# Kernel optimization log

Hardware: AMD Instinct MI355X
Metric: run time of the kernel (lower is better)

Reference implementation:

```python
import jax, jax.numpy as jnp
import numpy as np

N_IN = 1024
N_OUT = 1024
L, B = 2048, 16


def setup_inputs() -> dict:
    key = jax.random.key(0)
    k1, k2 = jax.random.split(key, 2)
    val = (3.0 / N_IN) ** 0.5  # matches init_weight uniform range
    return {
        "x": jax.random.normal(k1, (L, B, N_IN), dtype=jnp.float32),
        "c0": jnp.zeros((B, N_OUT), dtype=jnp.float32),
        "weight": jax.random.uniform(k2, (N_IN, 3 * N_OUT), dtype=jnp.float32, minval=-val, maxval=val),
        "bias": jnp.zeros((2 * N_OUT,), dtype=jnp.float32),
    }


def reference(x, c0, weight, bias):
    # x: (L, B, n_in); weight: (n_in, 3*n_out); bias: (2*n_out,)
    Lx, Bx, _ = x.shape
    # u_ = x @ W, viewed as (L, B, n_out, k=3); bidir=1 dropped
    u = (x.reshape(Lx * Bx, N_IN) @ weight).reshape(Lx, Bx, N_OUT, 3)
    x_tilde = u[..., 0]                                  # (L, B, d)
    forget = jax.nn.sigmoid(u[..., 1] + bias[:N_OUT])    # (L, B, d)
    # sequential SRU recurrence: c_t = (c_{t-1} - x~_t) * f_t + x~_t
    def step(c_prev, inputs):
        xt, ft = inputs
        c = (c_prev - xt) * ft + xt
        return c, c
    c_final, cs = jax.lax.scan(step, c0, (x_tilde, forget))
    h = jnp.tanh(cs)  # activation_type == 1 (tanh); no highway, no dropout (eval)
    return h, c_final
```

## Files before the change

kernel.cpp:

```cpp
#include <hip/hip_runtime.h>


typedef __attribute__((ext_vector_type(8))) short short8;
typedef __attribute__((ext_vector_type(4))) float f32x4;

#define L_SEQ 2048
#define BATCH 16
#define NIN   1024
#define NOUT  1024
#define MROWS (L_SEQ * BATCH)
#define NCOLS (2 * NOUT)
#define ROWELEMS (BATCH * NOUT)
#define NCHUNK 32
#define CHLEN  64
#define NT 16

__device__ __forceinline__ unsigned short f2bf(float f) {
  unsigned u = __float_as_uint(f);
  u += 0x7fffu + ((u >> 16) & 1u);
  return (unsigned short)(u >> 16);
}
__device__ __forceinline__ float bf2f(unsigned short b) {
  return __uint_as_float(((unsigned)b) << 16);
}
__device__ __forceinline__ float sigmoidf_(float x) {
  return __builtin_amdgcn_rcpf(1.f + __expf(-x));
}
__device__ __forceinline__ float fast_tanh(float x) {
  float ax = fabsf(x);
  float t = __expf(-2.f * ax);
  float r = (1.f - t) * __builtin_amdgcn_rcpf(1.f + t);
  return copysignf(r, x);
}

#define GLL16(gptr, lptr)                                              \
  __builtin_amdgcn_global_load_lds(                                    \
      (const __attribute__((address_space(1))) void*)(gptr),           \
      (__attribute__((address_space(3))) void*)(lptr), 16, 0, 0)

__global__ __launch_bounds__(256) void cvt_x_k(const float* __restrict__ x,
                                               unsigned short* __restrict__ o) {
  size_t i = ((size_t)blockIdx.x * 256 + threadIdx.x) * 8;
  const float4* p = (const float4*)(x + i);
  float4 a = p[0], b = p[1];
  union { unsigned short s[8]; uint4 v; } r;
  r.s[0] = f2bf(a.x); r.s[1] = f2bf(a.y); r.s[2] = f2bf(a.z); r.s[3] = f2bf(a.w);
  r.s[4] = f2bf(b.x); r.s[5] = f2bf(b.y); r.s[6] = f2bf(b.z); r.s[7] = f2bf(b.w);
  *(uint4*)(o + i) = r.v;
}

__global__ __launch_bounds__(256) void pack_w_k(const float* __restrict__ W,
                                                unsigned short* __restrict__ Bp) {
  __shared__ float tile[64][97];
  int n0 = blockIdx.x * 64;
  int k0 = blockIdx.y * 64;
  int c0 = 3 * (n0 >> 1);
  int tid = threadIdx.x;
  for (int idx = tid; idx < 64 * 96; idx += 256) {
    int r = idx / 96, c = idx - r * 96;
    tile[r][c] = W[(size_t)(k0 + r) * (3 * NOUT) + c0 + c];
  }
  __syncthreads();
#pragma unroll
  for (int q = 0; q < 2; ++q) {
    int pos = tid * 2 + q;
    int dn = pos >> 3;
    int j8 = (pos & 7) * 8;
    int cl = 3 * (dn >> 1) + (dn & 1);
    union { unsigned short s[8]; uint4 v; } r;
#pragma unroll
    for (int j = 0; j < 8; ++j) r.s[j] = f2bf(tile[j8 + j][cl]);
    *(uint4*)(Bp + (size_t)(n0 + dn) * NIN + k0 + j8) = r.v;
  }
}

#define BARR __builtin_amdgcn_s_barrier()
#define SCHED0 __builtin_amdgcn_sched_barrier(0)
#define VMCNT(n) asm volatile("s_waitcnt vmcnt(" #n ")" ::: "memory")

#define STAGE_A(bufc, ha, kt)                                                   \
  do {                                                                          \
    GLL16(pga##ha##0 + (kt) * 64, lds + (bufc) * 32768 + (ha) * 16384 + tid * 16);      \
    GLL16(pga##ha##1 + (kt) * 64, lds + (bufc) * 32768 + (ha) * 16384 + 8192 + tid * 16); \
  } while (0)
#define STAGE_B(bufc, hb, kt)                                                   \
  do {                                                                          \
    GLL16(pgb##hb##0 + (kt) * 64, lds + 65536 + (bufc) * 32768 + (hb) * 16384 + tid * 16); \
    GLL16(pgb##hb##1 + (kt) * 64, lds + 65536 + (bufc) * 32768 + (hb) * 16384 + 8192 + tid * 16); \
  } while (0)

#define LDA(DST, bufc, half)                                                    \
  _Pragma("unroll") for (int i = 0; i < 4; ++i) {                               \
    DST[i][0] = *(const short8*)(lds + (bufc) * 32768 + (half) * 16384 +        \
                                 (rowAb + i * 16) * 128 + colX0);               \
    DST[i][1] = *(const short8*)(lds + (bufc) * 32768 + (half) * 16384 +        \
                                 (rowAb + i * 16) * 128 + colX1);               \
  }
#define LDB(DST, bufc, half)                                                    \
  _Pragma("unroll") for (int j = 0; j < 2; ++j) {                               \
    DST[j][0] = *(const short8*)(lds + 65536 + (bufc) * 32768 + (half) * 16384 + \
                                 (rowBb + j * 16) * 128 + colX0);               \
    DST[j][1] = *(const short8*)(lds + 65536 + (bufc) * 32768 + (half) * 16384 + \
                                 (rowBb + j * 16) * 128 + colX1);               \
  }

#define MM(Q, AF, BF)                                                           \
  _Pragma("unroll") for (int i = 0; i < 4; ++i)                                 \
  _Pragma("unroll") for (int j = 0; j < 2; ++j) {                               \
    Q[i][j] = __builtin_amdgcn_mfma_f32_16x16x32_bf16(AF[i][0], BF[j][0], Q[i][j], 0, 0, 0); \
    Q[i][j] = __builtin_amdgcn_mfma_f32_16x16x32_bf16(AF[i][1], BF[j][1], Q[i][j], 0, 0, 0); \
  }

#define PH_TAIL(Q, AF, BF)                                                      \
  BARR;                                                                         \
  __builtin_amdgcn_s_setprio(1);                                                \
  MM(Q, AF, BF);                                                                \
  __builtin_amdgcn_s_setprio(0);                                                \
  BARR;                                                                         \
  SCHED0

#define PH_TAILV(Q, AF, BF)                                                     \
  BARR;                                                                         \
  __builtin_amdgcn_s_setprio(1);                                                \
  MM(Q, AF, BF);                                                                \
  __builtin_amdgcn_s_setprio(0);                                                \
  VMCNT(4);                                                                     \
  BARR;                                                                         \
  SCHED0

#define EPI(Q, qm, qn)                                                          \
  do {                                                                          \
    _Pragma("unroll") for (int i = 0; i < 4; ++i)                               \
    _Pragma("unroll") for (int j = 0; j < 2; ++j) {                             \
      int n = n0 + (qn) * 128 + wn * 32 + j * 16 + nc;                          \
      float bsel = bias[n >> 1];                                                \
      _Pragma("unroll") for (int r = 0; r < 4; ++r) {                           \
        int m = m0 + (qm) * 128 + wm * 64 + i * 16 + mr + r;                    \
        float v = Q[i][j][r];                                                   \
        if (isf) v = sigmoidf_(v + bsel);                                       \
        U[(size_t)m * NCOLS + n] = f2bf(v);                                     \
      }                                                                         \
    }                                                                           \
  } while (0)

__global__ __launch_bounds__(512, 2) void gemm8_k(const unsigned short* __restrict__ A,
                                                  const unsigned short* __restrict__ B,
                                                  const float* __restrict__ bias,
                                                  unsigned short* __restrict__ U) {
  __shared__ __align__(16) char lds[131072];
  const int K = NIN;
  int tid = threadIdx.x;
  int wave = tid >> 6;
  int lane = tid & 63;
  int wm = wave >> 2;
  int wn = wave & 3;
  int lr = lane & 15;
  int hi = lane >> 4;

  int bi = blockIdx.x;
  int t = (bi & 7) * 128 + (bi >> 3);
  int n0 = (t & 7) << 8;
  int m0 = (t >> 3) << 8;

  int rowAb = wm * 64 + lr;
  int rowBb = wn * 32 + lr;
  int swz = (lr & 7) << 4;
  int colX0 = (hi * 16) ^ swz;
  int colX1 = (64 + hi * 16) ^ swz;

  int row0 = tid >> 3;
  int gch = (tid & 7) ^ (row0 & 7);
  const unsigned short* pga00 = A + (size_t)(m0 + row0) * K + gch * 8;
  const unsigned short* pga01 = pga00 + (size_t)64 * K;
  const unsigned short* pga10 = pga00 + (size_t)128 * K;
  const unsigned short* pga11 = pga00 + (size_t)192 * K;
  const unsigned short* pgb00 = B + (size_t)(n0 + row0) * K + gch * 8;
  const unsigned short* pgb01 = pgb00 + (size_t)64 * K;
  const unsigned short* pgb10 = pgb00 + (size_t)128 * K;
  const unsigned short* pgb11 = pgb00 + (size_t)192 * K;

  f32x4 zero = {0.f, 0.f, 0.f, 0.f};
  f32x4 acc00[4][2], acc01[4][2], acc11[4][2], acc10[4][2];
#pragma unroll
  for (int i = 0; i < 4; ++i)
#pragma unroll
    for (int j = 0; j < 2; ++j) {
      acc00[i][j] = zero; acc01[i][j] = zero;
      acc11[i][j] = zero; acc10[i][j] = zero;
    }

  short8 af[4][2], bq0[2][2], bq1[2][2];

  STAGE_A(0, 0, 0); STAGE_A(0, 1, 0); STAGE_B(0, 0, 0); STAGE_B(0, 1, 0);
  STAGE_A(1, 0, 1); STAGE_B(1, 1, 1);
  VMCNT(4);
  BARR;
  SCHED0;

  for (int it = 0; it < NT / 2; ++it) {
    int kt = it * 2;
    int k1 = kt + 1, k2 = (kt + 2) & (NT - 1), k3 = (kt + 3) & (NT - 1);
    STAGE_B(1, 0, k1); STAGE_A(1, 1, k1);
    LDA(af, 0, 0); LDB(bq0, 0, 0);
    PH_TAIL(acc00, af, bq0);
    LDB(bq1, 0, 1);
    PH_TAIL(acc01, af, bq1);
    STAGE_A(0, 0, k2);
    LDA(af, 0, 1);
    PH_TAIL(acc11, af, bq1);
    STAGE_B(0, 1, k2);
    PH_TAILV(acc10, af, bq0);
    STAGE_A(0, 1, k2);
    LDA(af, 1, 0); LDB(bq0, 1, 0);
    PH_TAIL(acc00, af, bq0);
    STAGE_B(0, 0, k2);
    LDB(bq1, 1, 1);
    PH_TAIL(acc01, af, bq1);
    STAGE_A(1, 0, k3);
    LDA(af, 1, 1);
    PH_TAIL(acc11, af, bq1);
    STAGE_B(1, 1, k3);
    PH_TAILV(acc10, af, bq0);
  }
  VMCNT(0);

  int mr = hi * 4;
  int nc = lane & 15;
  bool isf = nc & 1;
  EPI(acc00, 0, 0);
  EPI(acc01, 0, 1);
  EPI(acc11, 1, 1);
  EPI(acc10, 1, 0);
}

__global__ __launch_bounds__(256) void scan_p1(const unsigned int* __restrict__ U2,
                                               float2* __restrict__ AV) {
  int tid = threadIdx.x;
  int bid = blockIdx.x;
  int bd = ((bid >> 7) << 10) + ((bid & 3) << 8) + tid;
  int chunk = (bid >> 2) & 31;
  const unsigned int* up = U2 + (size_t)chunk * CHLEN * ROWELEMS + bd;
  float a = 1.f, v = 0.f;
  for (int t0 = 0; t0 < CHLEN; t0 += 8) {
    unsigned int w[8];
#pragma unroll
    for (int j = 0; j < 8; ++j) w[j] = up[(size_t)(t0 + j) * ROWELEMS];
#pragma unroll
    for (int j = 0; j < 8; ++j) {
      float xt = bf2f((unsigned short)(w[j] & 0xffffu));
      float f  = bf2f((unsigned short)(w[j] >> 16));
      v = f * v + (1.f - f) * xt;
      a = a * f;
    }
  }
  AV[(size_t)chunk * ROWELEMS + bd] = make_float2(a, v);
}

__global__ __launch_bounds__(256) void scan_p2(const float2* __restrict__ AV,
                                               const float* __restrict__ c0,
                                               float* __restrict__ CS,
                                               float* __restrict__ out) {
  int bd = blockIdx.x * 256 + threadIdx.x;
  float c = c0[bd];
  float2 av[NCHUNK];
#pragma unroll
  for (int k = 0; k < NCHUNK; ++k) av[k] = AV[(size_t)k * ROWELEMS + bd];
#pragma unroll
  for (int k = 0; k < NCHUNK; ++k) {
    CS[(size_t)k * ROWELEMS + bd] = c;
    c = av[k].x * c + av[k].y;
  }
  out[(size_t)MROWS * NOUT + bd] = c;
}

__global__ __launch_bounds__(256) void scan_p3(const unsigned int* __restrict__ U2,
                                               const float* __restrict__ CS,
                                               float* __restrict__ out) {
  int tid = threadIdx.x;
  int bid = blockIdx.x;
  int bd = ((bid >> 7) << 10) + ((bid & 3) << 8) + tid;
  int chunk = (bid >> 2) & 31;
  float c = CS[(size_t)chunk * ROWELEMS + bd];
  const unsigned int* up = U2 + (size_t)chunk * CHLEN * ROWELEMS + bd;
  float* op = out + (size_t)chunk * CHLEN * ROWELEMS + bd;
  for (int t0 = 0; t0 < CHLEN; t0 += 8) {
    unsigned int w[8];
#pragma unroll
    for (int j = 0; j < 8; ++j) w[j] = up[(size_t)(t0 + j) * ROWELEMS];
#pragma unroll
    for (int j = 0; j < 8; ++j) {
      float xt = bf2f((unsigned short)(w[j] & 0xffffu));
      float f  = bf2f((unsigned short)(w[j] >> 16));
      c = (c - xt) * f + xt;
      op[(size_t)(t0 + j) * ROWELEMS] = fast_tanh(c);
    }
  }
}

extern "C" void kernel_launch(void* const* d_in, const int* in_sizes, int n_in,
                              void* d_out, int out_size, void* d_ws, size_t ws_size,
                              hipStream_t stream) {
  const float* x    = (const float*)d_in[0];
  const float* c0   = (const float*)d_in[1];
  const float* W    = (const float*)d_in[2];
  const float* bias = (const float*)d_in[3];
  float* out = (float*)d_out;

  char* ws = (char*)d_ws;
  unsigned short* Abf = (unsigned short*)ws;
  unsigned short* Bp  = (unsigned short*)(ws + ((size_t)64 << 20));
  unsigned short* U   = (unsigned short*)(ws + ((size_t)68 << 20));
  float2* AV = (float2*)ws;
  float*  CS = (float*)(ws + ((size_t)4 << 20));

  cvt_x_k<<<MROWS * NIN / (256 * 8), 256, 0, stream>>>(x, Abf);
  pack_w_k<<<dim3(NCOLS / 64, NIN / 64), 256, 0, stream>>>(W, Bp);
  gemm8_k<<<1024, 512, 0, stream>>>(Abf, Bp, bias, U);
  scan_p1<<<2048, 256, 0, stream>>>((const unsigned int*)U, AV);
  scan_p2<<<64, 256, 0, stream>>>(AV, c0, CS, out);
  scan_p3<<<2048, 256, 0, stream>>>((const unsigned int*)U, CS, out);
}
```

Before: 254.2 us.

## Merge GEMM phases into paired MFMA blocks and peel the final k-iteration

```diff
diff --git a/kernel.cpp b/kernel.cpp
--- a/kernel.cpp
+++ b/kernel.cpp
@@ -111,20 +111,32 @@
     Q[i][j] = __builtin_amdgcn_mfma_f32_16x16x32_bf16(AF[i][1], BF[j][1], Q[i][j], 0, 0, 0); \
   }
 
-#define PH_TAIL(Q, AF, BF)                                                      \
+#define PH2_TAIL(Q1, BF1, Q2, BF2)                                              \
   BARR;                                                                         \
   __builtin_amdgcn_s_setprio(1);                                                \
-  MM(Q, AF, BF);                                                                \
+  MM(Q1, af, BF1);                                                              \
+  MM(Q2, af, BF2);                                                              \
   __builtin_amdgcn_s_setprio(0);                                                \
   BARR;                                                                         \
   SCHED0
 
-#define PH_TAILV(Q, AF, BF)                                                     \
+#define PH2_TAILV(Q1, BF1, Q2, BF2)                                             \
   BARR;                                                                         \
   __builtin_amdgcn_s_setprio(1);                                                \
-  MM(Q, AF, BF);                                                                \
+  MM(Q1, af, BF1);                                                              \
+  MM(Q2, af, BF2);                                                              \
   __builtin_amdgcn_s_setprio(0);                                                \
   VMCNT(4);                                                                     \
+  BARR;                                                                         \
+  SCHED0
+
+#define PH2_TAILV0(Q1, BF1, Q2, BF2)                                            \
+  BARR;                                                                         \
+  __builtin_amdgcn_s_setprio(1);                                                \
+  MM(Q1, af, BF1);                                                              \
+  MM(Q2, af, BF2);                                                              \
+  __builtin_amdgcn_s_setprio(0);                                                \
+  VMCNT(0);                                                                     \
   BARR;                                                                         \
   SCHED0
 
@@ -197,32 +209,34 @@
   BARR;
   SCHED0;
 
-  for (int it = 0; it < NT / 2; ++it) {
+  for (int it = 0; it < NT / 2 - 1; ++it) {
     int kt = it * 2;
-    int k1 = kt + 1, k2 = (kt + 2) & (NT - 1), k3 = (kt + 3) & (NT - 1);
+    int k1 = kt + 1, k2 = kt + 2, k3 = kt + 3;
     STAGE_B(1, 0, k1); STAGE_A(1, 1, k1);
-    LDA(af, 0, 0); LDB(bq0, 0, 0);
-    PH_TAIL(acc00, af, bq0);
-    LDB(bq1, 0, 1);
-    PH_TAIL(acc01, af, bq1);
-    STAGE_A(0, 0, k2);
+    LDA(af, 0, 0); LDB(bq0, 0, 0); LDB(bq1, 0, 1);
+    PH2_TAIL(acc00, bq0, acc01, bq1);
+    STAGE_A(0, 0, k2); STAGE_B(0, 1, k2);
     LDA(af, 0, 1);
-    PH_TAIL(acc11, af, bq1);
-    STAGE_B(0, 1, k2);
-    PH_TAILV(acc10, af, bq0);
-    STAGE_A(0, 1, k2);
-    LDA(af, 1, 0); LDB(bq0, 1, 0);
-    PH_TAIL(acc00, af, bq0);
-    STAGE_B(0, 0, k2);
-    LDB(bq1, 1, 1);
-    PH_TAIL(acc01, af, bq1);
-    STAGE_A(1, 0, k3);
+    PH2_TAILV(acc11, bq1, acc10, bq0);
+    STAGE_A(0, 1, k2); STAGE_B(0, 0, k2);
+    LDA(af, 1, 0); LDB(bq0, 1, 0); LDB(bq1, 1, 1);
+    PH2_TAIL(acc00, bq0, acc01, bq1);
+    STAGE_A(1, 0, k3); STAGE_B(1, 1, k3);
     LDA(af, 1, 1);
-    PH_TAIL(acc11, af, bq1);
-    STAGE_B(1, 1, k3);
-    PH_TAILV(acc10, af, bq0);
-  }
-  VMCNT(0);
+    PH2_TAILV(acc11, bq1, acc10, bq0);
+  }
+
+  {
+    STAGE_B(1, 0, 15); STAGE_A(1, 1, 15);
+    LDA(af, 0, 0); LDB(bq0, 0, 0); LDB(bq1, 0, 1);
+    PH2_TAIL(acc00, bq0, acc01, bq1);
+    LDA(af, 0, 1);
+    PH2_TAILV0(acc11, bq1, acc10, bq0);
+    LDA(af, 1, 0); LDB(bq0, 1, 0); LDB(bq1, 1, 1);
+    PH2_TAIL(acc00, bq0, acc01, bq1);
+    LDA(af, 1, 1);
+    PH2_TAIL(acc11, bq1, acc10, bq0);
+  }
 
   int mr = hi * 4;
   int nc = lane & 15;
```

Result: no change. 251.2 us, median of 2 (-1.2%).
